# Kernel optimization log

Measured on AMD Instinct MI355X. Metric: run time of the kernel, lower is better.

## Reference

```python
import jax, jax.numpy as jnp
import numpy as np

B, IN_DIM, R_DIM = 8192, 2048, 4096
LEAK_RATE = 0.3


def setup_inputs() -> dict:
    key = jax.random.key(0)
    k1, k2, k3, k4 = jax.random.split(key, 4)
    inputs = jax.random.normal(k1, (B, IN_DIM), dtype=jnp.float32)
    prev_state = jax.random.normal(k2, (B, R_DIM), dtype=jnp.float32)
    # weights scaled down for numerical sanity inside tanh
    input_weights = jax.random.normal(k3, (R_DIM, IN_DIM), dtype=jnp.float32) * 0.02
    reservoir_weights = jax.random.normal(k4, (R_DIM, R_DIM), dtype=jnp.float32) * 0.02
    return {
        "inputs": inputs,
        "prev_state": prev_state,
        "input_weights": input_weights,
        "reservoir_weights": reservoir_weights,
    }


def reference(inputs, prev_state, input_weights, reservoir_weights):
    # input_part = inputs @ input_weights.T        -> [B, R]
    # reservoir_part = prev_state @ reservoir_weights.T -> [B, R]
    input_part = jnp.einsum("bi,ri->br", inputs, input_weights)
    reservoir_part = jnp.einsum("bq,rq->br", prev_state, reservoir_weights)
    state = (1.0 - LEAK_RATE) * prev_state + LEAK_RATE * jnp.tanh(input_part + reservoir_part)
    return state
```

## Files before the change

kernel.cpp:

```cpp
#include <hip/hip_runtime.h>
#include <cstdint>
#include <cstddef>

typedef unsigned short u16;
typedef __attribute__((ext_vector_type(8))) short short8;
typedef __attribute__((ext_vector_type(4))) float f32x4;
typedef __attribute__((ext_vector_type(4))) int i32x4;

constexpr int M  = 8192;
constexpr int Nn = 4096;
constexpr int K1 = 2048;
constexpr int K2 = 4096;
constexpr int K  = K1 + K2;
constexpr int BM = 256, BN = 256;
constexpr int NKT = K / 64;
constexpr float LEAK = 0.3f;

__device__ __forceinline__ u16 f2bf(float f) {
  unsigned u = __float_as_uint(f);
  u += 0x7FFFu + ((u >> 16) & 1u);
  return (u16)(u >> 16);
}

template<int C1, int C2>
__global__ void cast_concat(const float* __restrict__ X, const float* __restrict__ S,
                            u16* __restrict__ out, int rows)
{
  constexpr int C = C1 + C2;
  const size_t total = (size_t)rows * C / 8;
  for (size_t i = blockIdx.x * (size_t)blockDim.x + threadIdx.x; i < total;
       i += (size_t)gridDim.x * blockDim.x) {
    const size_t e = i * 8;
    const int r = (int)(e / C);
    const int c = (int)(e - (size_t)r * C);
    const float* src = (c < C1) ? (X + (size_t)r * C1 + c)
                                : (S + (size_t)r * C2 + (c - C1));
    const float4* s4 = (const float4*)src;
    float4 f0 = s4[0], f1 = s4[1];
    alignas(16) u16 tmp[8];
    tmp[0] = f2bf(f0.x); tmp[1] = f2bf(f0.y); tmp[2] = f2bf(f0.z); tmp[3] = f2bf(f0.w);
    tmp[4] = f2bf(f1.x); tmp[5] = f2bf(f1.y); tmp[6] = f2bf(f1.z); tmp[7] = f2bf(f1.w);
    *(i32x4*)(out + e) = *(i32x4*)tmp;
  }
}

__device__ __forceinline__ void gload16(const u16* g, u16* l) {
  __builtin_amdgcn_global_load_lds(
      (const __attribute__((address_space(1))) void*)g,
      (__attribute__((address_space(3))) void*)l, 16, 0, 0);
}

__device__ __forceinline__ float fast_tanh(float x) {
  const float ax = __builtin_fabsf(x);
  const float e  = __builtin_amdgcn_exp2f(ax * 2.8853900817779268f);
  const float r  = 1.0f - 2.0f * __builtin_amdgcn_rcpf(e + 1.0f);
  return __builtin_copysignf(r, x);
}

#define BAR()   __builtin_amdgcn_s_barrier()
#define LGKM0() asm volatile("s_waitcnt lgkmcnt(0)" ::: "memory")
#define VMW4()  asm volatile("s_waitcnt vmcnt(4)" ::: "memory")
#define VMW0()  asm volatile("s_waitcnt vmcnt(0)" ::: "memory")
#define SB0()   __builtin_amdgcn_sched_barrier(0)

__global__ __launch_bounds__(512, 2) void gemm_fused(
    const u16* __restrict__ A,
    const u16* __restrict__ W,
    const float* __restrict__ prev,
    float* __restrict__ out)
{
  __shared__ u16 lds[65536];

  const int tid  = threadIdx.x;
  const int lane = tid & 63;
  const int wid  = tid >> 6;
  const int wr   = wid >> 2;
  const int wc   = wid & 3;

  const int cpx = gridDim.x >> 3;
  const int wg  = ((int)blockIdx.x & 7) * cpx + ((int)blockIdx.x >> 3);
  const int bn  = wg & 15;
  const int bm  = wg >> 4;

  const int sr = tid >> 3;
  const int ss = (tid & 7) ^ (sr & 7);
  const u16* pA = A + (size_t)(bm * BM + sr) * K + ss * 8;
  const u16* pW = W + (size_t)(bn * BN + sr) * K + ss * 8;
  u16* ldsw = lds + wid * 512;
  const size_t rowK64  = (size_t)64  * K;
  const size_t rowK128 = (size_t)128 * K;

  auto stg = [&](const u16* g, int dst) {
    gload16(g,          ldsw + dst);
    gload16(g + rowK64, ldsw + dst + 4096);
  };

  const int fr  = lane & 15;
  const int khi = lane >> 4;
  const int lx  = lane & 7;
  const int aoff0 = wr * 8192 + fr * 64 + ((khi    ) ^ lx) * 8;
  const int aoff1 = wr * 8192 + fr * 64 + ((4 + khi) ^ lx) * 8;
  const int brow  = (wc & 1) * 64 + fr;
  const int boff0 = (wc >> 1) * 8192 + brow * 64 + ((khi    ) ^ lx) * 8;
  const int boff1 = (wc >> 1) * 8192 + brow * 64 + ((4 + khi) ^ lx) * 8;

  short8 af[4][2], bf[4][2];
  f32x4  acc[8][4];
  #pragma unroll
  for (int m = 0; m < 8; ++m)
    #pragma unroll
    for (int n = 0; n < 4; ++n) acc[m][n] = (f32x4)0.f;

  auto dsA = [&](int mg, int ab) {
    #pragma unroll
    for (int mi = 0; mi < 4; ++mi) {
      af[mi][0] = *(const short8*)(lds + ab + aoff0 + (mg * 4 + mi) * 1024);
      af[mi][1] = *(const short8*)(lds + ab + aoff1 + (mg * 4 + mi) * 1024);
    }
  };
  auto dsB = [&](int ng, int bb) {
    #pragma unroll
    for (int ni = 0; ni < 2; ++ni) {
      const int n = ng * 2 + ni;
      bf[n][0] = *(const short8*)(lds + bb + boff0 + n * 1024);
      bf[n][1] = *(const short8*)(lds + bb + boff1 + n * 1024);
    }
  };
  auto MM = [&](int mg, int ng) {
    __builtin_amdgcn_s_setprio(1);
    #pragma unroll
    for (int ni = 0; ni < 2; ++ni)
      #pragma unroll
      for (int mi = 0; mi < 4; ++mi)
        #pragma unroll
        for (int ks = 0; ks < 2; ++ks)
          acc[mg * 4 + mi][ng * 2 + ni] = __builtin_amdgcn_mfma_f32_16x16x32_bf16(
              af[mi][ks], bf[ng * 2 + ni][ks], acc[mg * 4 + mi][ng * 2 + ni], 0, 0, 0);
    __builtin_amdgcn_s_setprio(0);
  };

  stg(pW,                32768);
  stg(pW + rowK128,      32768 + 8192);
  stg(pA,                0);
  stg(pA + rowK128,      8192);
  stg(pW + 64,           49152);
  stg(pW + 64 + rowK128, 49152 + 8192);
  VMW4();
  BAR();

  const u16* gA = pA;
  const u16* gW = pW;
  #pragma unroll 1
  for (int i = 0; i < NKT / 2 - 1; ++i) {
    dsA(0, 0); dsB(0, 32768);
    stg(gA + 64, 16384);
    BAR(); LGKM0(); SB0(); MM(0, 0); BAR();
    dsB(1, 32768);
    stg(gA + 64 + rowK128, 16384 + 8192);
    BAR(); LGKM0(); SB0(); MM(0, 1); BAR();
    dsA(1, 0);
    stg(gW + 128, 32768);
    BAR(); LGKM0(); SB0(); MM(1, 0); BAR();
    stg(gW + 128 + rowK128, 32768 + 8192);
    BAR(); MM(1, 1); VMW4(); BAR();
    dsA(0, 16384); dsB(0, 49152);
    stg(gA + 128, 0);
    BAR(); LGKM0(); SB0(); MM(0, 0); BAR();
    dsB(1, 49152);
    stg(gA + 128 + rowK128, 8192);
    BAR(); LGKM0(); SB0(); MM(0, 1); BAR();
    dsA(1, 16384);
    stg(gW + 192, 49152);
    BAR(); LGKM0(); SB0(); MM(1, 0); BAR();
    stg(gW + 192 + rowK128, 49152 + 8192);
    BAR(); MM(1, 1); VMW4(); BAR();
    gA += 128; gW += 128;
  }

  dsA(0, 0); dsB(0, 32768);
  stg(gA + 64, 16384);
  BAR(); LGKM0(); SB0(); MM(0, 0); BAR();
  dsB(1, 32768);
  stg(gA + 64 + rowK128, 16384 + 8192);
  BAR(); LGKM0(); SB0(); MM(0, 1); BAR();
  dsA(1, 0);
  BAR(); LGKM0(); SB0(); MM(1, 0); BAR();
  BAR(); MM(1, 1); VMW0(); BAR();
  dsA(0, 16384); dsB(0, 49152);
  BAR(); LGKM0(); SB0(); MM(0, 0); BAR();
  dsB(1, 49152);
  BAR(); LGKM0(); SB0(); MM(0, 1); BAR();
  dsA(1, 16384);
  BAR(); LGKM0(); SB0(); MM(1, 0); BAR();
  BAR(); MM(1, 1);

  const int crow0 = bm * BM + wr * 128 + khi * 4;
  const int ccol0 = bn * BN + wc * 64 + fr;
  #pragma unroll
  for (int m = 0; m < 8; ++m)
    #pragma unroll
    for (int n = 0; n < 4; ++n)
      #pragma unroll
      for (int j = 0; j < 4; ++j) {
        const int row = crow0 + m * 16 + j;
        const size_t off = (size_t)row * Nn + ccol0 + n * 16;
        out[off] = (1.0f - LEAK) * prev[off] + LEAK * fast_tanh(acc[m][n][j]);
      }
}

extern "C" void kernel_launch(void* const* d_in, const int* in_sizes, int n_in,
                              void* d_out, int out_size, void* d_ws, size_t ws_size,
                              hipStream_t stream) {
  const float* inputs = (const float*)d_in[0];
  const float* prev   = (const float*)d_in[1];
  const float* w_in   = (const float*)d_in[2];
  const float* w_res  = (const float*)d_in[3];
  float* out = (float*)d_out;

  u16* Acat = (u16*)d_ws;
  u16* Wcat = Acat + (size_t)M * K;

  cast_concat<K1, K2><<<2048, 256, 0, stream>>>(inputs, prev, Acat, M);
  cast_concat<K1, K2><<<1024, 256, 0, stream>>>(w_in, w_res, Wcat, Nn);

  gemm_fused<<<(M / BM) * (Nn / BN), 512, 0, stream>>>(Acat, Wcat, prev, out);
}
```

Baseline: 433.6 us.

## Double-buffer MFMA fragments and overlap LDS reads with compute in GEMM loop

Splits the A and B register fragments into even/odd buffers so LDS reads for the next sub-tile are issued before the current MFMA block, using partial lgkmcnt/vmcnt waits instead of full drains. Barriers per step are reduced and the global-to-LDS staging order is reshuffled into a deeper software pipeline. The aim is to hide LDS latency and barrier stalls behind MFMA work, at the cost of more VGPR pressure under the 512x2 launch bounds and delicate wait-count correctness.

New measurement: 431.3 us. About the same (-0.5%).

```diff
diff --git a/kernel.cpp b/kernel.cpp
--- a/kernel.cpp
+++ b/kernel.cpp
@@ -59,6 +59,9 @@
 
 #define BAR()   __builtin_amdgcn_s_barrier()
 #define LGKM0() asm volatile("s_waitcnt lgkmcnt(0)" ::: "memory")
+#define LGKM4() asm volatile("s_waitcnt lgkmcnt(4)" ::: "memory")
+#define LGKM8() asm volatile("s_waitcnt lgkmcnt(8)" ::: "memory")
+#define VMW2()  asm volatile("s_waitcnt vmcnt(2)" ::: "memory")
 #define VMW4()  asm volatile("s_waitcnt vmcnt(4)" ::: "memory")
 #define VMW0()  asm volatile("s_waitcnt vmcnt(0)" ::: "memory")
 #define SB0()   __builtin_amdgcn_sched_barrier(0)
@@ -104,29 +107,29 @@
   const int boff0 = (wc >> 1) * 8192 + brow * 64 + ((khi    ) ^ lx) * 8;
   const int boff1 = (wc >> 1) * 8192 + brow * 64 + ((4 + khi) ^ lx) * 8;
 
-  short8 af[4][2], bf[4][2];
+  short8 afE[4][2], afO[4][2];
+  short8 bfE[2][2], bfO[2][2];
   f32x4  acc[8][4];
   #pragma unroll
   for (int m = 0; m < 8; ++m)
     #pragma unroll
     for (int n = 0; n < 4; ++n) acc[m][n] = (f32x4)0.f;
 
-  auto dsA = [&](int mg, int ab) {
+  auto dsA = [&](short8 (&Av)[4][2], int mg, int ab) {
     #pragma unroll
     for (int mi = 0; mi < 4; ++mi) {
-      af[mi][0] = *(const short8*)(lds + ab + aoff0 + (mg * 4 + mi) * 1024);
-      af[mi][1] = *(const short8*)(lds + ab + aoff1 + (mg * 4 + mi) * 1024);
+      Av[mi][0] = *(const short8*)(lds + ab + aoff0 + (mg * 4 + mi) * 1024);
+      Av[mi][1] = *(const short8*)(lds + ab + aoff1 + (mg * 4 + mi) * 1024);
     }
   };
-  auto dsB = [&](int ng, int bb) {
+  auto dsB = [&](short8 (&Bv)[2][2], int ng, int bb) {
     #pragma unroll
     for (int ni = 0; ni < 2; ++ni) {
-      const int n = ng * 2 + ni;
-      bf[n][0] = *(const short8*)(lds + bb + boff0 + n * 1024);
-      bf[n][1] = *(const short8*)(lds + bb + boff1 + n * 1024);
+      Bv[ni][0] = *(const short8*)(lds + bb + boff0 + (ng * 2 + ni) * 1024);
+      Bv[ni][1] = *(const short8*)(lds + bb + boff1 + (ng * 2 + ni) * 1024);
     }
   };
-  auto MM = [&](int mg, int ng) {
+  auto MM = [&](short8 (&Av)[4][2], short8 (&Bv)[2][2], int mg, int ng) {
     __builtin_amdgcn_s_setprio(1);
     #pragma unroll
     for (int ni = 0; ni < 2; ++ni)
@@ -135,64 +138,68 @@
         #pragma unroll
         for (int ks = 0; ks < 2; ++ks)
           acc[mg * 4 + mi][ng * 2 + ni] = __builtin_amdgcn_mfma_f32_16x16x32_bf16(
-              af[mi][ks], bf[ng * 2 + ni][ks], acc[mg * 4 + mi][ng * 2 + ni], 0, 0, 0);
+              Av[mi][ks], Bv[ni][ks], acc[mg * 4 + mi][ng * 2 + ni], 0, 0, 0);
     __builtin_amdgcn_s_setprio(0);
   };
 
-  stg(pW,                32768);
-  stg(pW + rowK128,      32768 + 8192);
-  stg(pA,                0);
-  stg(pA + rowK128,      8192);
-  stg(pW + 64,           49152);
-  stg(pW + 64 + rowK128, 49152 + 8192);
+  stg(pA,            0);
+  stg(pA + rowK128,  8192);
+  stg(pW,            32768);
+  stg(pW + rowK128,  32768 + 8192);
+  stg(pW + 64,       49152);
+  stg(pA + 64,       16384);
   VMW4();
   BAR();
+  dsA(afE, 0, 0);
+  dsB(bfE, 0, 32768);
 
   const u16* gA = pA;
   const u16* gW = pW;
   #pragma unroll 1
-  for (int i = 0; i < NKT / 2 - 1; ++i) {
-    dsA(0, 0); dsB(0, 32768);
-    stg(gA + 64, 16384);
-    BAR(); LGKM0(); SB0(); MM(0, 0); BAR();
-    dsB(1, 32768);
+  for (int i = 0; i < 47; ++i) {
+    dsB(bfO, 1, 32768);
     stg(gA + 64 + rowK128, 16384 + 8192);
-    BAR(); LGKM0(); SB0(); MM(0, 1); BAR();
-    dsA(1, 0);
+    LGKM4(); SB0(); MM(afE, bfE, 0, 0); BAR();
+    dsA(afO, 1, 0);
+    stg(gW + 64 + rowK128, 49152 + 8192);
+    LGKM8(); SB0(); MM(afE, bfO, 0, 1); VMW2(); BAR();
+    dsA(afE, 0, 16384);
     stg(gW + 128, 32768);
-    BAR(); LGKM0(); SB0(); MM(1, 0); BAR();
+    LGKM8(); SB0(); MM(afO, bfE, 1, 0); VMW2(); BAR();
+    dsB(bfE, 0, 49152);
+    stg(gA + 128, 0);
+    SB0(); MM(afO, bfO, 1, 1); BAR();
+    dsB(bfO, 1, 49152);
+    stg(gA + 128 + rowK128, 8192);
+    LGKM4(); SB0(); MM(afE, bfE, 0, 0); BAR();
+    dsA(afO, 1, 16384);
     stg(gW + 128 + rowK128, 32768 + 8192);
-    BAR(); MM(1, 1); VMW4(); BAR();
-    dsA(0, 16384); dsB(0, 49152);
-    stg(gA + 128, 0);
-    BAR(); LGKM0(); SB0(); MM(0, 0); BAR();
-    dsB(1, 49152);
-    stg(gA + 128 + rowK128, 8192);
-    BAR(); LGKM0(); SB0(); MM(0, 1); BAR();
-    dsA(1, 16384);
+    LGKM8(); SB0(); MM(afE, bfO, 0, 1); VMW2(); BAR();
+    dsA(afE, 0, 0);
     stg(gW + 192, 49152);
-    BAR(); LGKM0(); SB0(); MM(1, 0); BAR();
-    stg(gW + 192 + rowK128, 49152 + 8192);
-    BAR(); MM(1, 1); VMW4(); BAR();
+    LGKM8(); SB0(); MM(afO, bfE, 1, 0); VMW2(); BAR();
+    dsB(bfE, 0, 32768);
+    stg(gA + 192, 16384);
+    SB0(); MM(afO, bfO, 1, 1); BAR();
     gA += 128; gW += 128;
   }
 
-  dsA(0, 0); dsB(0, 32768);
-  stg(gA + 64, 16384);
-  BAR(); LGKM0(); SB0(); MM(0, 0); BAR();
-  dsB(1, 32768);
+  dsB(bfO, 1, 32768);
   stg(gA + 64 + rowK128, 16384 + 8192);
-  BAR(); LGKM0(); SB0(); MM(0, 1); BAR();
-  dsA(1, 0);
-  BAR(); LGKM0(); SB0(); MM(1, 0); BAR();
-  BAR(); MM(1, 1); VMW0(); BAR();
-  dsA(0, 16384); dsB(0, 49152);
-  BAR(); LGKM0(); SB0(); MM(0, 0); BAR();
-  dsB(1, 49152);
-  BAR(); LGKM0(); SB0(); MM(0, 1); BAR();
-  dsA(1, 16384);
-  BAR(); LGKM0(); SB0(); MM(1, 0); BAR();
-  BAR(); MM(1, 1);
+  LGKM4(); SB0(); MM(afE, bfE, 0, 0); BAR();
+  dsA(afO, 1, 0);
+  stg(gW + 64 + rowK128, 49152 + 8192);
+  LGKM8(); SB0(); MM(afE, bfO, 0, 1); VMW2(); BAR();
+  dsA(afE, 0, 16384);
+  LGKM8(); SB0(); MM(afO, bfE, 1, 0); VMW0(); BAR();
+  dsB(bfE, 0, 49152);
+  SB0(); MM(afO, bfO, 1, 1); BAR();
+  dsB(bfO, 1, 49152);
+  LGKM4(); SB0(); MM(afE, bfE, 0, 0); BAR();
+  dsA(afO, 1, 16384);
+  LGKM8(); SB0(); MM(afE, bfO, 0, 1); BAR();
+  LGKM0(); SB0(); MM(afO, bfE, 1, 0);
+  MM(afO, bfO, 1, 1);
 
   const int crow0 = bm * BM + wr * 128 + khi * 4;
   const int ccol0 = bn * BN + wc * 64 + fr;
```
